# Kernel optimization log

Measured on AMD Instinct MI355X. Metric: run time of the kernel, lower is better.

Reference implementation:

```python
import jax, jax.numpy as jnp
import numpy as np

NUM_EMBEDDINGS = 1024
EMBEDDING_DIM = 128
COMMITMENT_COST = 0.25


def setup_inputs() -> dict:
    key = jax.random.key(0)
    k1, k2 = jax.random.split(key)
    z = jax.random.normal(k1, (16, EMBEDDING_DIM, 64, 64), dtype=jnp.float32)
    # torch init: uniform(-1/num_embeddings, 1/num_embeddings)
    lim = 1.0 / NUM_EMBEDDINGS
    embedding = jax.random.uniform(
        k2, (NUM_EMBEDDINGS, EMBEDDING_DIM), dtype=jnp.float32,
        minval=-lim, maxval=lim)
    return {"z": z, "embedding": embedding}


def reference(z, embedding):
    b, c, h, w = z.shape  # c == EMBEDDING_DIM
    # (b, h, w, c) -> (b*h*w, c)
    z_flat = jnp.transpose(z, (0, 2, 3, 1)).reshape(-1, c)
    # squared euclidean distances: ||z||^2 + ||e||^2 - 2 z e^T  -> (N, K)
    distances = (jnp.sum(z_flat ** 2, axis=-1, keepdims=True)
                 + jnp.sum(embedding ** 2, axis=-1)[None, :]
                 - 2.0 * jnp.matmul(z_flat, embedding.T))
    encoding_indices = jnp.argmin(distances, axis=-1)  # (N,) int
    z_q = embedding[encoding_indices].reshape(b, h, w, c)
    z_q = jnp.transpose(z_q, (0, 3, 1, 2))  # (b, c, h, w)
    commitment_loss = COMMITMENT_COST * jnp.sum(
        (jax.lax.stop_gradient(z_q) - z) ** 2)
    codebook_loss = jnp.sum((z_q - jax.lax.stop_gradient(z)) ** 2)
    loss = codebook_loss + commitment_loss
    # straight-through estimator
    z_q_st = z + jax.lax.stop_gradient(z_q - z)
    return (z_q_st, loss, encoding_indices, commitment_loss, codebook_loss)
```

## Files before the change

kernel.cpp:

```cpp
#include <hip/hip_runtime.h>
#include <hip/hip_bf16.h>

#define C 128
#define HW 4096
#define NPOS 65536
#define K 1024
#define MB 128
#define NBLK (NPOS/MB)
#define RS 136
#define CHK 64
#define NCH (K/CHK)
#define IMG_RS 256
#define CHB (CHK*IMG_RS)

#define ZQ_OFF 0
#define LOSS_OFF 8388608
#define IDX_OFF 8388609
#define COMMIT_OFF 8454145
#define CODE_OFF 8454146

#define WS_EN_OFF 256
#define WS_IMG_OFF 8192

typedef __bf16 bf16x8 __attribute__((ext_vector_type(8)));
typedef float f32x4 __attribute__((ext_vector_type(4)));

__global__ void vq_prep(const float* __restrict__ emb, unsigned char* __restrict__ img,
                        float* __restrict__ enorm1) {
    int t = threadIdx.x;
    int r = t >> 5, l = t & 31;
    int k = blockIdx.x * 8 + r;
    float4 v = ((const float4*)emb)[k * 32 + l];
    __hip_bfloat16 h0 = __float2bfloat16(v.x), h1 = __float2bfloat16(v.y),
                   h2 = __float2bfloat16(v.z), h3 = __float2bfloat16(v.w);
    ushort4 pk;
    pk.x = *(unsigned short*)&h0; pk.y = *(unsigned short*)&h1;
    pk.z = *(unsigned short*)&h2; pk.w = *(unsigned short*)&h3;
    *(ushort4*)(img + (size_t)k * IMG_RS + l * 8) = pk;
    float s = v.x * v.x + v.y * v.y + v.z * v.z + v.w * v.w;
    #pragma unroll
    for (int off = 16; off; off >>= 1) s += __shfl_xor(s, off);
    if (l == 0) enorm1[k] = s + 1.0f;
}

__global__ __launch_bounds__(256, 2)
void vq_main(const float* __restrict__ z, const float* __restrict__ emb,
             const unsigned char* __restrict__ img, const float* __restrict__ enorm1,
             float* __restrict__ out, float* __restrict__ S, unsigned int* __restrict__ cnt) {
    __shared__ unsigned short zt[MB * RS];
    __shared__ unsigned int wbest[4][MB];
    __shared__ unsigned short idxs[MB];
    __shared__ float lred[4];

    const int t = threadIdx.x;
    const int w = t >> 6;
    const int lane = t & 63;
    const int nn = lane & 15;
    const int q = lane >> 4;

    const int n0g = blockIdx.x * MB;
    const int b = n0g >> 12;
    const int hw0 = n0g & (HW - 1);
    const float* zg = z + (size_t)b * C * HW + hw0;

    {
        int pos = t & (MB - 1);
        int c0b = (t >> 7) * 64;
        #pragma unroll
        for (int i = 0; i < 16; ++i) {
            int c0 = c0b + i * 4;
            float f0 = zg[(size_t)(c0 + 0) * HW + pos];
            float f1 = zg[(size_t)(c0 + 1) * HW + pos];
            float f2 = zg[(size_t)(c0 + 2) * HW + pos];
            float f3 = zg[(size_t)(c0 + 3) * HW + pos];
            __hip_bfloat16 h0 = __float2bfloat16(f0), h1 = __float2bfloat16(f1),
                           h2 = __float2bfloat16(f2), h3 = __float2bfloat16(f3);
            ushort4 pk;
            pk.x = *(unsigned short*)&h0; pk.y = *(unsigned short*)&h1;
            pk.z = *(unsigned short*)&h2; pk.w = *(unsigned short*)&h3;
            *(ushort4*)&zt[pos * RS + c0] = pk;
        }
    }
    __syncthreads();

    bf16x8 a[8][4];
    #pragma unroll
    for (int mt = 0; mt < 8; ++mt)
        #pragma unroll
        for (int ks = 0; ks < 4; ++ks)
            a[mt][ks] = *(bf16x8*)&zt[(mt * 16 + nn) * RS + ks * 32 + q * 8];

    unsigned int best[8][4];
    #pragma unroll
    for (int mt = 0; mt < 8; ++mt)
        #pragma unroll
        for (int r = 0; r < 4; ++r) best[mt][r] = 0xFFFFFFFFu;

    const unsigned char* gB = img + (size_t)(w * 16 + nn) * IMG_RS + q * 16;
    const float* gE = enorm1 + w * 16 + nn;

    bf16x8 bcur[4], bnxt[4];
    #pragma unroll
    for (int ks = 0; ks < 4; ++ks)
        bcur[ks] = *(const bf16x8*)(gB + ks * 64);

    for (int ch = 0; ch < NCH; ++ch) {
        if (ch + 1 < NCH) {
            const unsigned char* src = gB + (size_t)(ch + 1) * CHB;
            #pragma unroll
            for (int ks = 0; ks < 4; ++ks)
                bnxt[ks] = *(const bf16x8*)(src + ks * 64);
        }
        const float en1 = gE[ch * CHK];
        const unsigned int code = (unsigned int)(ch * CHK + w * 16 + nn);

        f32x4 acc[8];
        #pragma unroll
        for (int mt = 0; mt < 8; ++mt) acc[mt] = (f32x4){0.f, 0.f, 0.f, 0.f};
        #pragma unroll
        for (int ks = 0; ks < 4; ++ks)
            #pragma unroll
            for (int mt = 0; mt < 8; ++mt)
                acc[mt] = __builtin_amdgcn_mfma_f32_16x16x32_bf16(a[mt][ks], bcur[ks], acc[mt], 0, 0, 0);

        #pragma unroll
        for (int mt = 0; mt < 8; ++mt)
            #pragma unroll
            for (int r = 0; r < 4; ++r) {
                float s = fmaf(acc[mt][r], -2.0f, en1);
                unsigned int u = (__float_as_uint(s) & ~1023u) | code;
                best[mt][r] = min(best[mt][r], u);
            }
        #pragma unroll
        for (int ks = 0; ks < 4; ++ks) bcur[ks] = bnxt[ks];
    }

    #pragma unroll
    for (int mt = 0; mt < 8; ++mt)
        #pragma unroll
        for (int r = 0; r < 4; ++r) {
            unsigned int v = best[mt][r];
            v = min(v, (unsigned int)__shfl_xor((int)v, 1));
            v = min(v, (unsigned int)__shfl_xor((int)v, 2));
            v = min(v, (unsigned int)__shfl_xor((int)v, 4));
            v = min(v, (unsigned int)__shfl_xor((int)v, 8));
            if (nn == 0) wbest[w][mt * 16 + q * 4 + r] = v;
        }
    __syncthreads();

    if (t < MB) {
        unsigned int v = min(min(wbest[0][t], wbest[1][t]), min(wbest[2][t], wbest[3][t]));
        unsigned int code = v & 1023u;
        idxs[t] = (unsigned short)code;
        out[IDX_OFF + n0g + t] = (float)code;
    }
    __syncthreads();

    {
        int pos = t & (MB - 1);
        int c0b = (t >> 7) * 64;
        int myidx = idxs[pos];
        const float* erow = emb + (size_t)myidx * C;
        float* og = out + ZQ_OFF + (size_t)b * C * HW + hw0;
        float ls = 0.f;
        #pragma unroll
        for (int i = 0; i < 16; ++i) {
            int c0 = c0b + i * 4;
            float4 ev = *(const float4*)&erow[c0];
            ushort4 zz = *(ushort4*)&zt[pos * RS + c0];
            float z0 = __uint_as_float((unsigned int)zz.x << 16);
            float z1 = __uint_as_float((unsigned int)zz.y << 16);
            float z2 = __uint_as_float((unsigned int)zz.z << 16);
            float z3 = __uint_as_float((unsigned int)zz.w << 16);
            float d0 = z0 - ev.x, d1 = z1 - ev.y, d2 = z2 - ev.z, d3 = z3 - ev.w;
            ls += d0 * d0 + d1 * d1 + d2 * d2 + d3 * d3;
            og[(size_t)(c0 + 0) * HW + pos] = ev.x;
            og[(size_t)(c0 + 1) * HW + pos] = ev.y;
            og[(size_t)(c0 + 2) * HW + pos] = ev.z;
            og[(size_t)(c0 + 3) * HW + pos] = ev.w;
        }
        #pragma unroll
        for (int off = 32; off; off >>= 1) ls += __shfl_down(ls, off);
        if (lane == 0) lred[w] = ls;
    }
    __syncthreads();

    if (t == 0) {
        atomicAdd(S, lred[0] + lred[1] + lred[2] + lred[3]);
        __threadfence();
        unsigned int old = atomicAdd(cnt, 1u);
        if (old == NBLK - 1) {
            float s = atomicAdd(S, 0.0f);
            out[LOSS_OFF] = 1.25f * s;
            out[COMMIT_OFF] = 0.25f * s;
            out[CODE_OFF] = s;
        }
    }
}

extern "C" void kernel_launch(void* const* d_in, const int* in_sizes, int n_in,
                              void* d_out, int out_size, void* d_ws, size_t ws_size,
                              hipStream_t stream) {
    const float* z = (const float*)d_in[0];
    const float* emb = (const float*)d_in[1];
    float* out = (float*)d_out;
    float* S = (float*)d_ws;
    unsigned int* cnt = (unsigned int*)d_ws + 1;
    float* enorm1 = (float*)((unsigned char*)d_ws + WS_EN_OFF);
    unsigned char* img = (unsigned char*)d_ws + WS_IMG_OFF;

    hipMemsetAsync(d_ws, 0, 64, stream);
    vq_prep<<<K / 8, 256, 0, stream>>>(emb, img, enorm1);
    vq_main<<<NBLK, 256, 0, stream>>>(z, emb, img, enorm1, out, S, cnt);
}
```

Before: 131.6 us.

## Halve position tile, split codebook across waves, gather bf16 codebook for output

Block tile shrinks from 128 to 64 positions, doubling the grid, and occupancy is raised to 3 blocks per CU. Each wave now scans a contiguous quarter of the codebook (256 codes) with 4 M-tiles, where before all waves strided over the whole codebook with 8 M-tiles. The output z_q is gathered from the bf16 codebook image instead of the fp32 embedding, which cuts gather bytes but writes bf16-rounded codebook values to the output and the loss. The aim is more parallelism and lower register pressure per wave, at the cost of loading each B fragment for fewer A rows.

```diff
diff --git a/kernel.cpp b/kernel.cpp
--- a/kernel.cpp
+++ b/kernel.cpp
@@ -5,13 +5,10 @@
 #define HW 4096
 #define NPOS 65536
 #define K 1024
-#define MB 128
+#define MB 64
 #define NBLK (NPOS/MB)
 #define RS 136
-#define CHK 64
-#define NCH (K/CHK)
 #define IMG_RS 256
-#define CHB (CHK*IMG_RS)
 
 #define ZQ_OFF 0
 #define LOSS_OFF 8388608
@@ -43,8 +40,8 @@
     if (l == 0) enorm1[k] = s + 1.0f;
 }
 
-__global__ __launch_bounds__(256, 2)
-void vq_main(const float* __restrict__ z, const float* __restrict__ emb,
+__global__ __launch_bounds__(256, 3)
+void vq_main(const float* __restrict__ z,
              const unsigned char* __restrict__ img, const float* __restrict__ enorm1,
              float* __restrict__ out, float* __restrict__ S, unsigned int* __restrict__ cnt) {
     __shared__ unsigned short zt[MB * RS];
@@ -64,10 +61,10 @@
     const float* zg = z + (size_t)b * C * HW + hw0;
 
     {
-        int pos = t & (MB - 1);
-        int c0b = (t >> 7) * 64;
-        #pragma unroll
-        for (int i = 0; i < 16; ++i) {
+        int pos = t & 63;
+        int c0b = (t >> 6) * 32;
+        #pragma unroll
+        for (int i = 0; i < 8; ++i) {
             int c0 = c0b + i * 4;
             float f0 = zg[(size_t)(c0 + 0) * HW + pos];
             float f1 = zg[(size_t)(c0 + 1) * HW + pos];
@@ -83,48 +80,49 @@
     }
     __syncthreads();
 
-    bf16x8 a[8][4];
-    #pragma unroll
-    for (int mt = 0; mt < 8; ++mt)
+    bf16x8 a[4][4];
+    #pragma unroll
+    for (int mt = 0; mt < 4; ++mt)
         #pragma unroll
         for (int ks = 0; ks < 4; ++ks)
             a[mt][ks] = *(bf16x8*)&zt[(mt * 16 + nn) * RS + ks * 32 + q * 8];
 
-    unsigned int best[8][4];
-    #pragma unroll
-    for (int mt = 0; mt < 8; ++mt)
+    unsigned int best[4][4];
+    #pragma unroll
+    for (int mt = 0; mt < 4; ++mt)
         #pragma unroll
         for (int r = 0; r < 4; ++r) best[mt][r] = 0xFFFFFFFFu;
 
-    const unsigned char* gB = img + (size_t)(w * 16 + nn) * IMG_RS + q * 16;
-    const float* gE = enorm1 + w * 16 + nn;
+    const int base_w = w * 256;
+    const unsigned char* gB = img + (size_t)(base_w + nn) * IMG_RS + q * 16;
+    const float* gE = enorm1 + base_w + nn;
 
     bf16x8 bcur[4], bnxt[4];
     #pragma unroll
     for (int ks = 0; ks < 4; ++ks)
         bcur[ks] = *(const bf16x8*)(gB + ks * 64);
 
-    for (int ch = 0; ch < NCH; ++ch) {
-        if (ch + 1 < NCH) {
-            const unsigned char* src = gB + (size_t)(ch + 1) * CHB;
+    for (int cc = 0; cc < 16; ++cc) {
+        if (cc + 1 < 16) {
+            const unsigned char* src = gB + (size_t)(cc + 1) * 16 * IMG_RS;
             #pragma unroll
             for (int ks = 0; ks < 4; ++ks)
                 bnxt[ks] = *(const bf16x8*)(src + ks * 64);
         }
-        const float en1 = gE[ch * CHK];
-        const unsigned int code = (unsigned int)(ch * CHK + w * 16 + nn);
-
-        f32x4 acc[8];
-        #pragma unroll
-        for (int mt = 0; mt < 8; ++mt) acc[mt] = (f32x4){0.f, 0.f, 0.f, 0.f};
+        const float en1 = gE[cc * 16];
+        const unsigned int code = (unsigned int)(base_w + cc * 16 + nn);
+
+        f32x4 acc[4];
+        #pragma unroll
+        for (int mt = 0; mt < 4; ++mt) acc[mt] = (f32x4){0.f, 0.f, 0.f, 0.f};
         #pragma unroll
         for (int ks = 0; ks < 4; ++ks)
             #pragma unroll
-            for (int mt = 0; mt < 8; ++mt)
+            for (int mt = 0; mt < 4; ++mt)
                 acc[mt] = __builtin_amdgcn_mfma_f32_16x16x32_bf16(a[mt][ks], bcur[ks], acc[mt], 0, 0, 0);
 
         #pragma unroll
-        for (int mt = 0; mt < 8; ++mt)
+        for (int mt = 0; mt < 4; ++mt)
             #pragma unroll
             for (int r = 0; r < 4; ++r) {
                 float s = fmaf(acc[mt][r], -2.0f, en1);
@@ -136,7 +134,7 @@
     }
 
     #pragma unroll
-    for (int mt = 0; mt < 8; ++mt)
+    for (int mt = 0; mt < 4; ++mt)
         #pragma unroll
         for (int r = 0; r < 4; ++r) {
             unsigned int v = best[mt][r];
@@ -157,27 +155,28 @@
     __syncthreads();
 
     {
-        int pos = t & (MB - 1);
-        int c0b = (t >> 7) * 64;
+        int pos = t & 63;
+        int c0b = (t >> 6) * 32;
         int myidx = idxs[pos];
-        const float* erow = emb + (size_t)myidx * C;
+        const unsigned char* brow = img + (size_t)myidx * IMG_RS + c0b * 2;
         float* og = out + ZQ_OFF + (size_t)b * C * HW + hw0;
         float ls = 0.f;
         #pragma unroll
-        for (int i = 0; i < 16; ++i) {
-            int c0 = c0b + i * 4;
-            float4 ev = *(const float4*)&erow[c0];
-            ushort4 zz = *(ushort4*)&zt[pos * RS + c0];
-            float z0 = __uint_as_float((unsigned int)zz.x << 16);
-            float z1 = __uint_as_float((unsigned int)zz.y << 16);
-            float z2 = __uint_as_float((unsigned int)zz.z << 16);
-            float z3 = __uint_as_float((unsigned int)zz.w << 16);
-            float d0 = z0 - ev.x, d1 = z1 - ev.y, d2 = z2 - ev.z, d3 = z3 - ev.w;
-            ls += d0 * d0 + d1 * d1 + d2 * d2 + d3 * d3;
-            og[(size_t)(c0 + 0) * HW + pos] = ev.x;
-            og[(size_t)(c0 + 1) * HW + pos] = ev.y;
-            og[(size_t)(c0 + 2) * HW + pos] = ev.z;
-            og[(size_t)(c0 + 3) * HW + pos] = ev.w;
+        for (int i = 0; i < 4; ++i) {
+            ushort4 e0 = *(const ushort4*)(brow + i * 16);
+            ushort4 e1 = *(const ushort4*)(brow + i * 16 + 8);
+            ushort4 z0 = *(ushort4*)&zt[pos * RS + c0b + i * 8];
+            ushort4 z1 = *(ushort4*)&zt[pos * RS + c0b + i * 8 + 4];
+            unsigned short es[8] = {e0.x, e0.y, e0.z, e0.w, e1.x, e1.y, e1.z, e1.w};
+            unsigned short zs[8] = {z0.x, z0.y, z0.z, z0.w, z1.x, z1.y, z1.z, z1.w};
+            #pragma unroll
+            for (int j = 0; j < 8; ++j) {
+                float ev = __uint_as_float((unsigned int)es[j] << 16);
+                float zv = __uint_as_float((unsigned int)zs[j] << 16);
+                float d = zv - ev;
+                ls += d * d;
+                og[(size_t)(c0b + i * 8 + j) * HW + pos] = ev;
+            }
         }
         #pragma unroll
         for (int off = 32; off; off >>= 1) ls += __shfl_down(ls, off);
@@ -211,5 +210,5 @@
 
     hipMemsetAsync(d_ws, 0, 64, stream);
     vq_prep<<<K / 8, 256, 0, stream>>>(emb, img, enorm1);
-    vq_main<<<NBLK, 256, 0, stream>>>(z, emb, img, enorm1, out, S, cnt);
+    vq_main<<<NBLK, 256, 0, stream>>>(z, img, enorm1, out, S, cnt);
 }
```

Result: slower. 164.5 us (+25.0%).
